# Performance work log

Hardware: AMD Instinct MI355X
Metric: run time of the kernel (lower is better)

Reference implementation:

```python
import jax, jax.numpy as jnp
import numpy as np

N, E, D = 50000, 800000, 128   # nodes, edges, input feature dim
HEADS, HC = 8, 16
H = HEADS * HC                 # 128 hidden width after concat
G, OUT = 64, 16                # graphs in batch, output classes
EPS_BN = 1e-5


def _gat_conv(x, src, dst, edge_attr, W, att_src, att_dst, We, att_edge, b):
    """PyG GATConv (concat=True, negative_slope=0.2, add_self_loops=True,
    fill_value='mean' for edge_attr, dropout inactive in eval)."""
    n = x.shape[0]
    # self-loop edge attr = per-node mean of incoming edge attrs
    ones = jnp.ones((src.shape[0], 1), x.dtype)
    deg = jax.ops.segment_sum(ones, dst, num_segments=n)
    ea_mean = jax.ops.segment_sum(edge_attr, dst, num_segments=n) / jnp.maximum(deg, 1.0)
    loop = jnp.arange(n, dtype=src.dtype)
    src_f = jnp.concatenate([src, loop])
    dst_f = jnp.concatenate([dst, loop])
    ea = jnp.concatenate([edge_attr, ea_mean])          # [E+N, 1]
    h = (x @ W).reshape(n, HEADS, HC)                   # [N, heads, hc]
    a_src = jnp.sum(h * att_src, axis=-1)               # [N, heads]
    a_dst = jnp.sum(h * att_dst, axis=-1)               # [N, heads]
    he = (ea @ We).reshape(-1, HEADS, HC)               # [E+N, heads, hc]
    a_e = jnp.sum(he * att_edge, axis=-1)               # [E+N, heads]
    alpha = jax.nn.leaky_relu(a_src[src_f] + a_dst[dst_f] + a_e, 0.2)
    # segment softmax over destination nodes
    amax = jax.ops.segment_max(alpha, dst_f, num_segments=n)
    ex = jnp.exp(alpha - amax[dst_f])
    denom = jax.ops.segment_sum(ex, dst_f, num_segments=n)
    coef = ex / (denom[dst_f] + 1e-16)                  # [E+N, heads]
    out = jax.ops.segment_sum(h[src_f] * coef[..., None], dst_f, num_segments=n)
    return out.reshape(n, H) + b


def setup_inputs() -> dict:
    key = jax.random.key(0)
    k = lambda i: jax.random.fold_in(key, i)
    nrm = lambda i, shape, s=0.1: jax.random.normal(k(i), shape, dtype=jnp.float32) * s
    inp = {
        "x": jax.random.normal(k(0), (N, D), dtype=jnp.float32),
        "edge_index": jax.random.randint(k(1), (2, E), 0, N, dtype=jnp.int32),
        "edge_weights": jax.random.normal(k(2), (E, 1), dtype=jnp.float32),
        "batch": jnp.sort(jax.random.randint(k(3), (N,), 0, G, dtype=jnp.int32)),
        "bn_gamma": jnp.ones((D,), jnp.float32),
        "bn_beta": jnp.zeros((D,), jnp.float32),
        "bn_mean": nrm(4, (D,)),
        "bn_var": jax.random.uniform(k(5), (D,), dtype=jnp.float32) + 0.5,
    }
    ci = 10
    for li, ind in [(1, D), (2, H), (3, H)]:
        inp[f"W{li}"] = nrm(ci, (ind, H)); ci += 1
        inp[f"att_src{li}"] = nrm(ci, (HEADS, HC)); ci += 1
        inp[f"att_dst{li}"] = nrm(ci, (HEADS, HC)); ci += 1
        inp[f"We{li}"] = nrm(ci, (1, H)); ci += 1
        inp[f"att_edge{li}"] = nrm(ci, (HEADS, HC)); ci += 1
        inp[f"b{li}"] = jnp.zeros((H,), jnp.float32)
    inp["Wl1"] = nrm(40, (H, 2 * HC)); inp["bl1"] = jnp.zeros((2 * HC,), jnp.float32)
    inp["Wl2"] = nrm(41, (2 * HC, OUT)); inp["bl2"] = jnp.zeros((OUT,), jnp.float32)
    return inp


def reference(x, edge_index, edge_weights, batch,
              bn_gamma, bn_beta, bn_mean, bn_var,
              W1, att_src1, att_dst1, We1, att_edge1, b1,
              W2, att_src2, att_dst2, We2, att_edge2, b2,
              W3, att_src3, att_dst3, We3, att_edge3, b3,
              Wl1, bl1, Wl2, bl2):
    src, dst = edge_index[0], edge_index[1]
    # BatchNorm (eval mode, running stats)
    h = (x - bn_mean) / jnp.sqrt(bn_var + EPS_BN) * bn_gamma + bn_beta
    h = jax.nn.relu(_gat_conv(h, src, dst, edge_weights, W1, att_src1, att_dst1, We1, att_edge1, b1))
    h = jax.nn.relu(_gat_conv(h, src, dst, edge_weights, W2, att_src2, att_dst2, We2, att_edge2, b2))
    h = _gat_conv(h, src, dst, edge_weights, W3, att_src3, att_dst3, We3, att_edge3, b3)
    g = jax.ops.segment_max(h, batch, num_segments=G)   # global max pool -> [G, H]
    g = jax.nn.relu(g @ Wl1 + bl1)
    # dropout p=0.5 is identity in eval mode
    return g @ Wl2 + bl2
```

## Files before the change

kernel.cpp:

```cpp
#include <hip/hip_runtime.h>
#include <math.h>

#define NN 50000
#define NE 800000
#define NH 8
#define HDIM 128
#define NG 64
#define PSPLIT 16
#define MAXD 64

typedef __attribute__((ext_vector_type(8))) short bf16x8;
typedef __attribute__((ext_vector_type(4))) float f32x4;

static __device__ __forceinline__ float lrelu02(float x){ return x > 0.f ? x : 0.2f*x; }
static __device__ __forceinline__ unsigned short f2bf(float f){
    unsigned u = __float_as_uint(f);
    unsigned r = (u + 0x7FFFu + ((u >> 16) & 1u)) >> 16;
    return (unsigned short)r;
}
static __device__ __forceinline__ float bf2f(unsigned short h){ return __uint_as_float((unsigned)h << 16); }
static __device__ __forceinline__ float bf_lo(unsigned v){ return __uint_as_float(v << 16); }
static __device__ __forceinline__ float bf_hi(unsigned v){ return __uint_as_float(v & 0xFFFF0000u); }

__global__ void k_prep0(const float* W1, const float* W2, const float* W3,
                        unsigned short* Wth, unsigned short* Wtl,
                        const float* We1, const float* ae1, const float* We2, const float* ae2,
                        const float* We3, const float* ae3, float* wev,
                        const float* gam, const float* bet, const float* mean, const float* var,
                        float* sc, float* sh){
    if (blockIdx.x == 192){
        int t = threadIdx.x;
        if (t < 128){
            float s = gam[t] * rsqrtf(var[t] + 1e-5f);
            sc[t] = s; sh[t] = bet[t] - mean[t] * s;
        } else if (t < 152){
            int q = t - 128; int l = q >> 3, hd = q & 7;
            const float* We = (l == 0) ? We1 : (l == 1) ? We2 : We3;
            const float* ae = (l == 0) ? ae1 : (l == 1) ? ae2 : ae3;
            float s = 0.f;
            for (int c = 0; c < 16; c++) s += We[hd*16+c] * ae[hd*16+c];
            wev[q] = s;
        }
        return;
    }
    int i = blockIdx.x*256 + threadIdx.x;
    int l = i >> 14, rem = i & 16383;
    int k = rem >> 7, n = rem & 127;
    const float* W = (l==0) ? W1 : (l==1) ? W2 : W3;
    float w = W[k*128 + n];
    unsigned short hi = f2bf(w);
    unsigned short lo = f2bf(w - bf2f(hi));
    Wth[l*16384 + n*128 + k] = hi;
    Wtl[l*16384 + n*128 + k] = lo;
}

__global__ void k_scatter(const int* srcp, const int* dstp, const float* ew,
                          unsigned* cnt, unsigned* slab){
    int i = blockIdx.x*256 + threadIdx.x;
    if (i >= NE) return;
    int d = dstp[i];
    float w = ew[i];
    unsigned rank = atomicAdd(&cnt[d], 1u);
    if (rank < MAXD){
        unsigned ent = (unsigned)srcp[i] | ((unsigned)f2bf(w) << 16);
        __builtin_nontemporal_store(ent, &slab[(size_t)d*MAXD + rank]);
    }
}

__global__ __launch_bounds__(256, 3) void k_gemm1(const float* A,
        const unsigned short* Wth, const unsigned short* Wtl,
        const float* sc, const float* sh,
        const float* att_s, const float* att_d,
        unsigned* Hb, float* a_src, float* a_dst, int M){
    __shared__ unsigned short Ah[64][132];
    __shared__ unsigned short Al[64][132];
    int t = threadIdx.x;
    int row0 = blockIdx.x * 64;
    int w = t >> 6, l = t & 63;
    int lr = l & 15, lg = l >> 4;

    {
        const float2* A2 = (const float2*)A;
        for (int i = 0; i < 16; i++){
            int idx2 = t + i*256;
            int r = idx2 >> 6, c2 = idx2 & 63;
            float2 v = make_float2(0.f, 0.f);
            if (row0 + r < M){
                v = A2[(size_t)(row0+r)*64 + c2];
                float2 s2 = ((const float2*)sc)[c2], h2 = ((const float2*)sh)[c2];
                v.x = v.x*s2.x + h2.x; v.y = v.y*s2.y + h2.y;
            }
            unsigned short h0 = f2bf(v.x), h1 = f2bf(v.y);
            unsigned short l0 = f2bf(v.x - bf2f(h0)), l1 = f2bf(v.y - bf2f(h1));
            ((unsigned*)&Ah[r][0])[c2] = (unsigned)h0 | ((unsigned)h1 << 16);
            ((unsigned*)&Al[r][0])[c2] = (unsigned)l0 | ((unsigned)l1 << 16);
        }
    }
    __syncthreads();

    f32x4 acc[4][2];
    #pragma unroll
    for (int m = 0; m < 4; m++){ acc[m][0] = (f32x4){0,0,0,0}; acc[m][1] = (f32x4){0,0,0,0}; }

    #pragma unroll
    for (int ks = 0; ks < 4; ks++){
        int kk = ks*32 + lg*8;
        bf16x8 bh0 = *(const bf16x8*)&Wth[((w*2+0)*16 + lr)*128 + kk];
        bf16x8 bl0 = *(const bf16x8*)&Wtl[((w*2+0)*16 + lr)*128 + kk];
        bf16x8 bh1 = *(const bf16x8*)&Wth[((w*2+1)*16 + lr)*128 + kk];
        bf16x8 bl1 = *(const bf16x8*)&Wtl[((w*2+1)*16 + lr)*128 + kk];
        #pragma unroll
        for (int m = 0; m < 4; m++){
            bf16x8 a_h = *(const bf16x8*)&Ah[m*16 + lr][kk];
            bf16x8 a_l = *(const bf16x8*)&Al[m*16 + lr][kk];
            acc[m][0] = __builtin_amdgcn_mfma_f32_16x16x32_bf16(a_h, bh0, acc[m][0], 0, 0, 0);
            acc[m][0] = __builtin_amdgcn_mfma_f32_16x16x32_bf16(a_h, bl0, acc[m][0], 0, 0, 0);
            acc[m][0] = __builtin_amdgcn_mfma_f32_16x16x32_bf16(a_l, bh0, acc[m][0], 0, 0, 0);
            acc[m][1] = __builtin_amdgcn_mfma_f32_16x16x32_bf16(a_h, bh1, acc[m][1], 0, 0, 0);
            acc[m][1] = __builtin_amdgcn_mfma_f32_16x16x32_bf16(a_h, bl1, acc[m][1], 0, 0, 0);
            acc[m][1] = __builtin_amdgcn_mfma_f32_16x16x32_bf16(a_l, bh1, acc[m][1], 0, 0, 0);
        }
    }

    float asv[2], adv[2];
    #pragma unroll
    for (int n = 0; n < 2; n++){
        asv[n] = att_s[(w*2+n)*16 + lr];
        adv[n] = att_d[(w*2+n)*16 + lr];
    }
    #pragma unroll
    for (int m = 0; m < 4; m++){
        #pragma unroll
        for (int n = 0; n < 2; n++){
            #pragma unroll
            for (int r = 0; r < 4; r++){
                float v = acc[m][n][r];
                float pv = __shfl_xor(v, 1);
                int row = row0 + m*16 + lg*4 + r;
                if (!(l & 1) && row < M){
                    unsigned d = (unsigned)f2bf(v) | ((unsigned)f2bf(pv) << 16);
                    Hb[(size_t)row*64 + w*16 + n*8 + (lr >> 1)] = d;
                }
            }
        }
    }
    #pragma unroll
    for (int m = 0; m < 4; m++){
        #pragma unroll
        for (int r = 0; r < 4; r++){
            int row = row0 + m*16 + lg*4 + r;
            #pragma unroll
            for (int n = 0; n < 2; n++){
                float ps = acc[m][n][r] * asv[n];
                float pd = acc[m][n][r] * adv[n];
                #pragma unroll
                for (int off = 1; off < 16; off <<= 1){
                    ps += __shfl_xor(ps, off);
                    pd += __shfl_xor(pd, off);
                }
                if (lr == 0 && row < M){
                    a_src[row*NH + w*2 + n] = ps;
                    a_dst[row*NH + w*2 + n] = pd;
                }
            }
        }
    }
}

__global__ __launch_bounds__(256, 3) void k_gemm_bf(const unsigned* A16,
        const unsigned short* Wth, const unsigned short* Wtl,
        const float* att_s, const float* att_d,
        unsigned* Hb, float* a_src, float* a_dst, int M){
    __shared__ unsigned short Ah[64][132];
    int t = threadIdx.x;
    int row0 = blockIdx.x * 64;
    int w = t >> 6, l = t & 63;
    int lr = l & 15, lg = l >> 4;

    for (int i = 0; i < 16; i++){
        int idx = t + i*256;
        int r = idx >> 6, c2 = idx & 63;
        unsigned v = 0;
        if (row0 + r < M) v = A16[(size_t)(row0+r)*64 + c2];
        ((unsigned*)&Ah[r][0])[c2] = v;
    }
    __syncthreads();

    f32x4 acc[4][2];
    #pragma unroll
    for (int m = 0; m < 4; m++){ acc[m][0] = (f32x4){0,0,0,0}; acc[m][1] = (f32x4){0,0,0,0}; }

    #pragma unroll
    for (int ks = 0; ks < 4; ks++){
        int kk = ks*32 + lg*8;
        bf16x8 bh0 = *(const bf16x8*)&Wth[((w*2+0)*16 + lr)*128 + kk];
        bf16x8 bl0 = *(const bf16x8*)&Wtl[((w*2+0)*16 + lr)*128 + kk];
        bf16x8 bh1 = *(const bf16x8*)&Wth[((w*2+1)*16 + lr)*128 + kk];
        bf16x8 bl1 = *(const bf16x8*)&Wtl[((w*2+1)*16 + lr)*128 + kk];
        #pragma unroll
        for (int m = 0; m < 4; m++){
            bf16x8 a_h = *(const bf16x8*)&Ah[m*16 + lr][kk];
            acc[m][0] = __builtin_amdgcn_mfma_f32_16x16x32_bf16(a_h, bh0, acc[m][0], 0, 0, 0);
            acc[m][0] = __builtin_amdgcn_mfma_f32_16x16x32_bf16(a_h, bl0, acc[m][0], 0, 0, 0);
            acc[m][1] = __builtin_amdgcn_mfma_f32_16x16x32_bf16(a_h, bh1, acc[m][1], 0, 0, 0);
            acc[m][1] = __builtin_amdgcn_mfma_f32_16x16x32_bf16(a_h, bl1, acc[m][1], 0, 0, 0);
        }
    }

    float asv[2], adv[2];
    #pragma unroll
    for (int n = 0; n < 2; n++){
        asv[n] = att_s[(w*2+n)*16 + lr];
        adv[n] = att_d[(w*2+n)*16 + lr];
    }
    #pragma unroll
    for (int m = 0; m < 4; m++){
        #pragma unroll
        for (int n = 0; n < 2; n++){
            #pragma unroll
            for (int r = 0; r < 4; r++){
                float v = acc[m][n][r];
                float pv = __shfl_xor(v, 1);
                int row = row0 + m*16 + lg*4 + r;
                if (!(l & 1) && row < M){
                    unsigned d = (unsigned)f2bf(v) | ((unsigned)f2bf(pv) << 16);
                    Hb[(size_t)row*64 + w*16 + n*8 + (lr >> 1)] = d;
                }
            }
        }
    }
    #pragma unroll
    for (int m = 0; m < 4; m++){
        #pragma unroll
        for (int r = 0; r < 4; r++){
            int row = row0 + m*16 + lg*4 + r;
            #pragma unroll
            for (int n = 0; n < 2; n++){
                float ps = acc[m][n][r] * asv[n];
                float pd = acc[m][n][r] * adv[n];
                #pragma unroll
                for (int off = 1; off < 16; off <<= 1){
                    ps += __shfl_xor(ps, off);
                    pd += __shfl_xor(pd, off);
                }
                if (lr == 0 && row < M){
                    a_src[row*NH + w*2 + n] = ps;
                    a_dst[row*NH + w*2 + n] = pd;
                }
            }
        }
    }
}

__global__ __launch_bounds__(256) void k_aggr(const unsigned* cnt, const unsigned* slab,
                       const float* a_src, const float* a_dst, const float* wev,
                       const unsigned* Hb, const float* bias, unsigned* Out16, int do_relu){
    int wid = threadIdx.x >> 6, lane = threadIdx.x & 63;
    int n = blockIdx.x*4 + wid;
    if (n >= NN) return;
    unsigned dgt = cnt[n];
    int dg = (int)(dgt < MAXD ? dgt : MAXD);
    int hd = lane >> 3;
    float ad = a_dst[n*NH + hd];
    float wh = wev[hd];
    unsigned vself = Hb[(size_t)n*64 + lane];
    float asn = a_src[n*NH + hd];
    float accL0=0.f, accH0=0.f, den0=0.f, accL1=0.f, accH1=0.f, den1=0.f;
    float easum = 0.f;
    const uint4* srow4 = (const uint4*)&slab[(size_t)n*MAXD];
    for (int base = 0; base < dg; base += 16){
        uint4 e0 = srow4[(base>>2)+0], e1 = srow4[(base>>2)+1];
        uint4 e2 = srow4[(base>>2)+2], e3 = srow4[(base>>2)+3];
        unsigned ent[16] = {e0.x,e0.y,e0.z,e0.w, e1.x,e1.y,e1.z,e1.w,
                            e2.x,e2.y,e2.z,e2.w, e3.x,e3.y,e3.z,e3.w};
        unsigned v[16];
        #pragma unroll
        for (int j = 0; j < 16; j++) v[j] = Hb[(size_t)(ent[j] & 0xFFFFu)*64 + lane];
        float as[16];
        #pragma unroll
        for (int j = 0; j < 16; j++) as[j] = a_src[(ent[j] & 0xFFFFu)*NH + hd];
        #pragma unroll
        for (int j = 0; j < 16; j++){
            float eaw = bf2f((unsigned short)(ent[j] >> 16));
            bool live = (base + j < dg);
            float c = live ? __expf(lrelu02(as[j] + ad + eaw*wh)) : 0.f;
            easum += live ? eaw : 0.f;
            if (j & 1){ den1 += c; accL1 += c*bf_lo(v[j]); accH1 += c*bf_hi(v[j]); }
            else      { den0 += c; accL0 += c*bf_lo(v[j]); accH0 += c*bf_hi(v[j]); }
        }
    }
    {
        float ea_self = easum / fmaxf((float)dgt, 1.f);
        float c = __expf(lrelu02(asn + ad + ea_self*wh));
        den0 += c; accL0 += c*bf_lo(vself); accH0 += c*bf_hi(vself);
    }
    float inv = 1.f / (den0 + den1 + 1e-16f);
    float2 bv = ((const float2*)bias)[lane];
    float o0 = (accL0 + accL1) * inv + bv.x;
    float o1 = (accH0 + accH1) * inv + bv.y;
    if (do_relu){ o0 = fmaxf(o0, 0.f); o1 = fmaxf(o1, 0.f); }
    Out16[(size_t)n*64 + lane] = (unsigned)f2bf(o0) | ((unsigned)f2bf(o1) << 16);
}

static __device__ int lower_bound_batch(const int* b, int v){
    int lo = 0, hi = NN;
    while (lo < hi){
        int mid = (lo + hi) >> 1;
        if (b[mid] < v) lo = mid + 1; else hi = mid;
    }
    return lo;
}

__global__ void k_pool1(const unsigned* A16, const int* batch, float* gpart){
    int g = blockIdx.x >> 4, s = blockIdx.x & (PSPLIT-1);
    int start = lower_bound_batch(batch, g);
    int end   = lower_bound_batch(batch, g + 1);
    int nrows = end - start;
    int chunk = (nrows + PSPLIT - 1) / PSPLIT;
    int rs = start + s*chunk;
    int re = rs + chunk; if (re > end) re = end;
    int c = threadIdx.x;
    float m0 = -INFINITY, m1 = -INFINITY;
    for (int r = rs; r < re; r++){
        unsigned v = A16[(size_t)r*64 + c];
        m0 = fmaxf(m0, bf_lo(v));
        m1 = fmaxf(m1, bf_hi(v));
    }
    ((float2*)&gpart[(size_t)blockIdx.x*HDIM])[c] = make_float2(m0, m1);
}

__global__ void k_pool2(const float* gpart, float* gp){
    int g = blockIdx.x, col = threadIdx.x;
    float m = -INFINITY;
    for (int s = 0; s < PSPLIT; s++)
        m = fmaxf(m, gpart[(size_t)(g*PSPLIT+s)*HDIM + col]);
    gp[g*HDIM + col] = m;
}

__global__ __launch_bounds__(256) void k_mlp(const float* gp, const float* Wl1, const float* bl1,
                      const float* Wl2, const float* bl2, float* out){
    __shared__ float gl[NG*HDIM];
    __shared__ float t1[NG*32];
    int t = threadIdx.x;
    for (int i = 0; i < 8; i++)
        ((float4*)gl)[t + i*256] = ((const float4*)gp)[t + i*256];
    __syncthreads();
    for (int i = 0; i < 8; i++){
        int o = t + i*256;
        int gi = o >> 5, j = o & 31;
        float s = bl1[j];
        for (int k = 0; k < 128; k++) s += gl[gi*128 + k] * Wl1[k*32 + j];
        t1[o] = fmaxf(s, 0.f);
    }
    __syncthreads();
    for (int i = 0; i < 4; i++){
        int o = t + i*256;
        int gi = o >> 4, j = o & 15;
        float s = bl2[j];
        for (int k = 0; k < 32; k++) s += t1[gi*32 + k] * Wl2[k*16 + j];
        out[o] = s;
    }
}

extern "C" void kernel_launch(void* const* d_in, const int* in_sizes, int n_in,
                              void* d_out, int out_size, void* d_ws, size_t ws_size,
                              hipStream_t stream){
    const float* x    = (const float*)d_in[0];
    const int*   ei   = (const int*)d_in[1];
    const float* ew   = (const float*)d_in[2];
    const int*   batch= (const int*)d_in[3];
    const float* bng  = (const float*)d_in[4];
    const float* bnb  = (const float*)d_in[5];
    const float* bnm  = (const float*)d_in[6];
    const float* bnv  = (const float*)d_in[7];
    const float* Wmat[3] = {(const float*)d_in[8],  (const float*)d_in[14], (const float*)d_in[20]};
    const float* asr[3]  = {(const float*)d_in[9],  (const float*)d_in[15], (const float*)d_in[21]};
    const float* adt[3]  = {(const float*)d_in[10], (const float*)d_in[16], (const float*)d_in[22]};
    const float* Wep[3]  = {(const float*)d_in[11], (const float*)d_in[17], (const float*)d_in[23]};
    const float* aep[3]  = {(const float*)d_in[12], (const float*)d_in[18], (const float*)d_in[24]};
    const float* bp[3]   = {(const float*)d_in[13], (const float*)d_in[19], (const float*)d_in[25]};
    const float* Wl1 = (const float*)d_in[26];
    const float* bl1 = (const float*)d_in[27];
    const float* Wl2 = (const float*)d_in[28];
    const float* bl2 = (const float*)d_in[29];

    char* p = (char*)d_ws;
    auto alloc = [&](size_t bytes)->char*{
        char* r = p; p += (bytes + 255) & ~(size_t)255; return r;
    };
    unsigned* Hb    = (unsigned*)alloc((size_t)NN*64*4);
    unsigned* A16   = (unsigned*)alloc((size_t)NN*64*4);
    float*    a_src = (float*)alloc((size_t)NN*NH*4);
    float*    a_dst = (float*)alloc((size_t)NN*NH*4);
    unsigned* cnt   = (unsigned*)alloc((size_t)NN*4);
    unsigned* slab  = (unsigned*)alloc((size_t)NN*MAXD*4);
    float*    wev   = (float*)alloc(24*4);
    float*    scv   = (float*)alloc(128*4);
    float*    shv   = (float*)alloc(128*4);
    unsigned short* Wth = (unsigned short*)alloc((size_t)3*16384*2);
    unsigned short* Wtl = (unsigned short*)alloc((size_t)3*16384*2);
    float*    gpart = (float*)alloc((size_t)NG*PSPLIT*HDIM*4);
    float*    gpool = (float*)alloc((size_t)NG*HDIM*4);

    const int* srcp = ei;
    const int* dstp = ei + NE;

    hipMemsetAsync(cnt, 0, (size_t)NN*4, stream);
    k_prep0<<<193, 256, 0, stream>>>(Wmat[0], Wmat[1], Wmat[2], Wth, Wtl,
                                     Wep[0], aep[0], Wep[1], aep[1], Wep[2], aep[2], wev,
                                     bng, bnb, bnm, bnv, scv, shv);
    k_scatter<<<(NE+255)/256, 256, 0, stream>>>(srcp, dstp, ew, cnt, slab);

    k_gemm1<<<(NN+63)/64, 256, 0, stream>>>(x, Wth, Wtl, scv, shv,
                                            asr[0], adt[0], Hb, a_src, a_dst, NN);
    k_aggr<<<(NN+3)/4, 256, 0, stream>>>(cnt, slab, a_src, a_dst, wev,
                                         Hb, bp[0], A16, 1);
    for (int l = 1; l < 3; l++){
        k_gemm_bf<<<(NN+63)/64, 256, 0, stream>>>(A16, Wth + l*16384, Wtl + l*16384,
                                                  asr[l], adt[l], Hb, a_src, a_dst, NN);
        k_aggr<<<(NN+3)/4, 256, 0, stream>>>(cnt, slab, a_src, a_dst, wev + l*8,
                                             Hb, bp[l], A16, (l < 2) ? 1 : 0);
    }
    k_pool1<<<NG*PSPLIT, 64, 0, stream>>>(A16, batch, gpart);
    k_pool2<<<NG, 128, 0, stream>>>(gpart, gpool);
    k_mlp<<<1, 256, 0, stream>>>(gpool, Wl1, bl1, Wl2, bl2, (float*)d_out);
}
```

Baseline: 329.8 us.

## Fuse edge scatter into first GEMM and dedupe attention exp in aggregation

Folds the count-buffer zeroing into the prep kernel and merges the edge scatter kernel with the first GEMM into a single launch, with blocks split by index range. This removes a memset and a kernel boundary so scatter and GEMM blocks can overlap. In the aggregation kernel, each lane now computes one attention coefficient per (edge, head) pair and broadcasts it with shuffles, instead of every lane gathering a_src and evaluating exp redundantly. This cuts gathers and transcendentals at the cost of extra cross-lane shuffles; the fused kernel inherits the GEMM's launch bounds and shared-memory footprint for its scatter blocks too.

```diff
diff --git a/kernel.cpp b/kernel.cpp
--- a/kernel.cpp
+++ b/kernel.cpp
@@ -8,6 +8,8 @@
 #define NG 64
 #define PSPLIT 16
 #define MAXD 64
+#define GEMMB 782
+#define SCATB 3125
 
 typedef __attribute__((ext_vector_type(8))) short bf16x8;
 typedef __attribute__((ext_vector_type(4))) float f32x4;
@@ -27,7 +29,12 @@
                         const float* We1, const float* ae1, const float* We2, const float* ae2,
                         const float* We3, const float* ae3, float* wev,
                         const float* gam, const float* bet, const float* mean, const float* var,
-                        float* sc, float* sh){
+                        float* sc, float* sh, unsigned* cnt){
+    if (blockIdx.x >= 193){
+        int i = (blockIdx.x - 193)*256 + threadIdx.x;
+        if (i < NN) cnt[i] = 0;
+        return;
+    }
     if (blockIdx.x == 192){
         int t = threadIdx.x;
         if (t < 128){
@@ -54,28 +61,27 @@
     Wtl[l*16384 + n*128 + k] = lo;
 }
 
-__global__ void k_scatter(const int* srcp, const int* dstp, const float* ew,
-                          unsigned* cnt, unsigned* slab){
-    int i = blockIdx.x*256 + threadIdx.x;
-    if (i >= NE) return;
-    int d = dstp[i];
-    float w = ew[i];
-    unsigned rank = atomicAdd(&cnt[d], 1u);
-    if (rank < MAXD){
-        unsigned ent = (unsigned)srcp[i] | ((unsigned)f2bf(w) << 16);
-        __builtin_nontemporal_store(ent, &slab[(size_t)d*MAXD + rank]);
-    }
-}
-
-__global__ __launch_bounds__(256, 3) void k_gemm1(const float* A,
-        const unsigned short* Wth, const unsigned short* Wtl,
-        const float* sc, const float* sh,
-        const float* att_s, const float* att_d,
+__global__ __launch_bounds__(256, 3) void k_fused1(
+        const int* srcp, const int* dstp, const float* ew, unsigned* cnt, unsigned* slab,
+        const float* A, const unsigned short* Wth, const unsigned short* Wtl,
+        const float* sc, const float* sh, const float* att_s, const float* att_d,
         unsigned* Hb, float* a_src, float* a_dst, int M){
     __shared__ unsigned short Ah[64][132];
     __shared__ unsigned short Al[64][132];
+    if (blockIdx.x < SCATB){
+        int i = blockIdx.x*256 + threadIdx.x;
+        if (i >= NE) return;
+        int d = dstp[i];
+        float w = ew[i];
+        unsigned rank = atomicAdd(&cnt[d], 1u);
+        if (rank < MAXD){
+            unsigned ent = (unsigned)srcp[i] | ((unsigned)f2bf(w) << 16);
+            __builtin_nontemporal_store(ent, &slab[(size_t)d*MAXD + rank]);
+        }
+        return;
+    }
     int t = threadIdx.x;
-    int row0 = blockIdx.x * 64;
+    int row0 = (blockIdx.x - SCATB) * 64;
     int w = t >> 6, l = t & 63;
     int lr = l & 15, lg = l >> 4;
 
@@ -261,13 +267,16 @@
     unsigned dgt = cnt[n];
     int dg = (int)(dgt < MAXD ? dgt : MAXD);
     int hd = lane >> 3;
-    float ad = a_dst[n*NH + hd];
-    float wh = wev[hd];
+    int slot = lane >> 3;
+    int headA = lane & 7;
+    float adA = a_dst[n*NH + headA];
+    float whA = wev[headA];
     unsigned vself = Hb[(size_t)n*64 + lane];
-    float asn = a_src[n*NH + hd];
-    float accL0=0.f, accH0=0.f, den0=0.f, accL1=0.f, accH1=0.f, den1=0.f;
-    float easum = 0.f;
-    const uint4* srow4 = (const uint4*)&slab[(size_t)n*MAXD];
+    float asnA = a_src[n*NH + headA];
+    float accL0=0.f, accH0=0.f, accL1=0.f, accH1=0.f, den0=0.f, den1=0.f;
+    float easumA = 0.f;
+    const unsigned* srow = &slab[(size_t)n*MAXD];
+    const uint4* srow4 = (const uint4*)srow;
     for (int base = 0; base < dg; base += 16){
         uint4 e0 = srow4[(base>>2)+0], e1 = srow4[(base>>2)+1];
         uint4 e2 = srow4[(base>>2)+2], e3 = srow4[(base>>2)+3];
@@ -276,24 +285,36 @@
         unsigned v[16];
         #pragma unroll
         for (int j = 0; j < 16; j++) v[j] = Hb[(size_t)(ent[j] & 0xFFFFu)*64 + lane];
-        float as[16];
-        #pragma unroll
-        for (int j = 0; j < 16; j++) as[j] = a_src[(ent[j] & 0xFFFFu)*NH + hd];
-        #pragma unroll
-        for (int j = 0; j < 16; j++){
-            float eaw = bf2f((unsigned short)(ent[j] >> 16));
-            bool live = (base + j < dg);
-            float c = live ? __expf(lrelu02(as[j] + ad + eaw*wh)) : 0.f;
-            easum += live ? eaw : 0.f;
-            if (j & 1){ den1 += c; accL1 += c*bf_lo(v[j]); accH1 += c*bf_hi(v[j]); }
-            else      { den0 += c; accL0 += c*bf_lo(v[j]); accH0 += c*bf_hi(v[j]); }
-        }
-    }
-    {
-        float ea_self = easum / fmaxf((float)dgt, 1.f);
-        float c = __expf(lrelu02(asn + ad + ea_self*wh));
-        den0 += c; accL0 += c*bf_lo(vself); accH0 += c*bf_hi(vself);
-    }
+        unsigned eA0 = srow[base + slot];
+        unsigned eA1 = srow[base + 8 + slot];
+        float ea0 = bf2f((unsigned short)(eA0 >> 16));
+        float ea1 = bf2f((unsigned short)(eA1 >> 16));
+        float as0 = a_src[(eA0 & 0xFFFFu)*NH + headA];
+        float as1 = a_src[(eA1 & 0xFFFFu)*NH + headA];
+        bool l0 = (base + slot) < dg, l1 = (base + 8 + slot) < dg;
+        float c0 = l0 ? __expf(lrelu02(as0 + adA + ea0*whA)) : 0.f;
+        float c1 = l1 ? __expf(lrelu02(as1 + adA + ea1*whA)) : 0.f;
+        easumA += (l0 ? ea0 : 0.f) + (l1 ? ea1 : 0.f);
+        #pragma unroll
+        for (int j = 0; j < 8; j++){
+            float cj = __shfl(c0, j*8 + hd);
+            if (j & 1){ den1 += cj; accL1 += cj*bf_lo(v[j]); accH1 += cj*bf_hi(v[j]); }
+            else      { den0 += cj; accL0 += cj*bf_lo(v[j]); accH0 += cj*bf_hi(v[j]); }
+        }
+        #pragma unroll
+        for (int j = 0; j < 8; j++){
+            float cj = __shfl(c1, j*8 + hd);
+            if (j & 1){ den1 += cj; accL1 += cj*bf_lo(v[8+j]); accH1 += cj*bf_hi(v[8+j]); }
+            else      { den0 += cj; accL0 += cj*bf_lo(v[8+j]); accH0 += cj*bf_hi(v[8+j]); }
+        }
+    }
+    easumA += __shfl_xor(easumA, 8);
+    easumA += __shfl_xor(easumA, 16);
+    easumA += __shfl_xor(easumA, 32);
+    float ea_self = easumA / fmaxf((float)dgt, 1.f);
+    float csA = __expf(lrelu02(asnA + adA + ea_self*whA));
+    float cs = __shfl(csA, hd);
+    den0 += cs; accL0 += cs*bf_lo(vself); accH0 += cs*bf_hi(vself);
     float inv = 1.f / (den0 + den1 + 1e-16f);
     float2 bv = ((const float2*)bias)[lane];
     float o0 = (accL0 + accL1) * inv + bv.x;
@@ -405,13 +426,11 @@
     const int* srcp = ei;
     const int* dstp = ei + NE;
 
-    hipMemsetAsync(cnt, 0, (size_t)NN*4, stream);
-    k_prep0<<<193, 256, 0, stream>>>(Wmat[0], Wmat[1], Wmat[2], Wth, Wtl,
+    k_prep0<<<193 + 196, 256, 0, stream>>>(Wmat[0], Wmat[1], Wmat[2], Wth, Wtl,
                                      Wep[0], aep[0], Wep[1], aep[1], Wep[2], aep[2], wev,
-                                     bng, bnb, bnm, bnv, scv, shv);
-    k_scatter<<<(NE+255)/256, 256, 0, stream>>>(srcp, dstp, ew, cnt, slab);
-
-    k_gemm1<<<(NN+63)/64, 256, 0, stream>>>(x, Wth, Wtl, scv, shv,
+                                     bng, bnb, bnm, bnv, scv, shv, cnt);
+    k_fused1<<<SCATB + GEMMB, 256, 0, stream>>>(srcp, dstp, ew, cnt, slab,
+                                            x, Wth, Wtl, scv, shv,
                                             asr[0], adt[0], Hb, a_src, a_dst, NN);
     k_aggr<<<(NN+3)/4, 256, 0, stream>>>(cnt, slab, a_src, a_dst, wev,
                                          Hb, bp[0], A16, 1);
```

Measured after the change: 318.9 us. 3.3% less time.
